# Optimization experiments

Measured on AMD Instinct MI355X. Metric: run time of the kernel, lower is better.

## Reference

```python
import jax, jax.numpy as jnp
import numpy as np


def setup_inputs() -> dict:
    key = jax.random.key(0)
    k0, k1 = jax.random.split(key)
    B, S, T = 32, 512, 128
    return {
        "crf_score_0": jax.random.normal(k0, (B, S + 1, T, T), dtype=jnp.float32),
        "crf_score_1": jax.random.normal(k1, (B, S + 1, T), dtype=jnp.float32),
        "sof": 126,
        "eof": 127,
    }


def reference(crf_score_0, crf_score_1, sof, eof):
    # crf_score_0: [B, S+1, T, T], crf_score_1: [B, S+1, T]
    # Initial scores (note: original multiplies, not adds, at step 0)
    forscores = crf_score_0[:, 0, sof, :] * crf_score_1[:, 0, :]  # [B, T]

    # Move seq axis first for scan: [S, B, T, T] and [S, B, T]
    c0 = jnp.moveaxis(crf_score_0[:, 1:], 0, 1)
    c1 = jnp.moveaxis(crf_score_1[:, 1:], 0, 1)

    def fwd_step(fs, xs):
        t0, t1 = xs  # [B, T, T], [B, T]
        # cur[b, i, j] = fs[b, i] + t1[b, j] + t0[b, i, j]
        cur = fs[:, :, None] + t1[:, None, :] + t0
        new_fs = jnp.max(cur, axis=1)            # [B, T]
        bp = jnp.argmax(cur, axis=1).astype(jnp.int32)  # [B, T]
        return new_fs, bp

    _, back_points = jax.lax.scan(fwd_step, forscores, (c0, c1))  # bps: [S, B, T]

    # Backtrack exactly as the original loop: pointer starts at bp[-1][:, eof],
    # then for idx = S-1 .. 0: pointer = bp[idx][b, pointer]; decode[:, idx] = pointer.
    ptr0 = back_points[-1][:, eof]  # [B]

    def bwd_step(ptr, bp_t):
        new = jnp.take_along_axis(bp_t, ptr[:, None], axis=1)[:, 0]
        return new, new

    _, dec = jax.lax.scan(bwd_step, ptr0, back_points, reverse=True)  # [S, B]
    return dec.T.astype(jnp.int32)  # [B, S] decoded label indices
```

## Files before the change

kernel.cpp:

```cpp
#include <hip/hip_runtime.h>


constexpr int S = 512;
constexpr int T = 128;

__global__ __launch_bounds__(1024, 1)
void viterbi_fused(const float* __restrict__ c0, const float* __restrict__ c1,
                   const int* __restrict__ sofp, const int* __restrict__ eofp,
                   int* __restrict__ out)
{
    __shared__ float fs[2][T];
    __shared__ float pmax[32][T];
    __shared__ int   parg[32][T];
    __shared__ unsigned char bp[S][T];

    const int b   = blockIdx.x;
    const int tid = (int)threadIdx.x;
    const int jq  = tid & 31;
    const int g   = tid >> 5;
    const int col = jq * 4;
    const int row = g * 4;

    const float* c0b = c0 + (size_t)b * (S + 1) * T * T;
    const float* c1b = c1 + (size_t)b * (S + 1) * T;

    if (tid < T) {
        const int sof = sofp[0];
        fs[0][tid] = c0b[(size_t)sof * T + tid] * c1b[tid];
    }
    __syncthreads();

    {
    }
    const float* t0p = c0b + (size_t)1 * T * T;
    const float* t1p = c1b + (size_t)1 * T;
    float4 a0 = *(const float4*)(t0p + (size_t)(row + 0) * T + col);
    float4 a1 = *(const float4*)(t0p + (size_t)(row + 1) * T + col);
    float4 a2 = *(const float4*)(t0p + (size_t)(row + 2) * T + col);
    float4 a3 = *(const float4*)(t0p + (size_t)(row + 3) * T + col);
    float4 tv = *(const float4*)(t1p + col);

    int p = 0;
    for (int s = 1; s <= S; ++s) {
        float4 b0 = make_float4(0.f,0.f,0.f,0.f), b1 = b0, b2 = b0, b3 = b0, bt = b0;
        if (s < S) {
            const float* n0 = c0b + (size_t)(s + 1) * T * T;
            const float* n1 = c1b + (size_t)(s + 1) * T;
            b0 = *(const float4*)(n0 + (size_t)(row + 0) * T + col);
            b1 = *(const float4*)(n0 + (size_t)(row + 1) * T + col);
            b2 = *(const float4*)(n0 + (size_t)(row + 2) * T + col);
            b3 = *(const float4*)(n0 + (size_t)(row + 3) * T + col);
            bt = *(const float4*)(n1 + col);
        }

        const float f0 = fs[p][row + 0];
        const float f1 = fs[p][row + 1];
        const float f2 = fs[p][row + 2];
        const float f3 = fs[p][row + 3];

        float bx, by, bz, bw; int ix, iy, iz, iw; float v;
        bx = (f0 + tv.x) + a0.x; ix = row;
        by = (f0 + tv.y) + a0.y; iy = row;
        bz = (f0 + tv.z) + a0.z; iz = row;
        bw = (f0 + tv.w) + a0.w; iw = row;

        v = (f1 + tv.x) + a1.x; if (v > bx) { bx = v; ix = row + 1; }
        v = (f1 + tv.y) + a1.y; if (v > by) { by = v; iy = row + 1; }
        v = (f1 + tv.z) + a1.z; if (v > bz) { bz = v; iz = row + 1; }
        v = (f1 + tv.w) + a1.w; if (v > bw) { bw = v; iw = row + 1; }

        v = (f2 + tv.x) + a2.x; if (v > bx) { bx = v; ix = row + 2; }
        v = (f2 + tv.y) + a2.y; if (v > by) { by = v; iy = row + 2; }
        v = (f2 + tv.z) + a2.z; if (v > bz) { bz = v; iz = row + 2; }
        v = (f2 + tv.w) + a2.w; if (v > bw) { bw = v; iw = row + 2; }

        v = (f3 + tv.x) + a3.x; if (v > bx) { bx = v; ix = row + 3; }
        v = (f3 + tv.y) + a3.y; if (v > by) { by = v; iy = row + 3; }
        v = (f3 + tv.z) + a3.z; if (v > bz) { bz = v; iz = row + 3; }
        v = (f3 + tv.w) + a3.w; if (v > bw) { bw = v; iw = row + 3; }

        *(float4*)&pmax[g][col] = make_float4(bx, by, bz, bw);
        *(int4*)  &parg[g][col] = make_int4(ix, iy, iz, iw);
        __syncthreads();

        if (tid < T) {
            float bb = pmax[0][tid];
            int   ii = parg[0][tid];
            #pragma unroll
            for (int gg = 1; gg < 32; ++gg) {
                float vv = pmax[gg][tid];
                if (vv > bb) { bb = vv; ii = parg[gg][tid]; }
            }
            fs[p ^ 1][tid] = bb;
            bp[s - 1][tid] = (unsigned char)ii;
        }
        __syncthreads();

        p ^= 1;
        a0 = b0; a1 = b1; a2 = b2; a3 = b3; tv = bt;
    }

    if (tid == 0) {
        const int eof = eofp[0];
        int ptr = bp[S - 1][eof];
        for (int idx = S - 1; idx >= 0; --idx) {
            ptr = bp[idx][ptr];
            out[(size_t)b * S + idx] = ptr;
        }
    }
}

extern "C" void kernel_launch(void* const* d_in, const int* in_sizes, int n_in,
                              void* d_out, int out_size, void* d_ws, size_t ws_size,
                              hipStream_t stream)
{
    const float* c0  = (const float*)d_in[0];
    const float* c1  = (const float*)d_in[1];
    const int*   sof = (const int*)d_in[2];
    const int*   eof = (const int*)d_in[3];
    int*         out = (int*)d_out;

    const int B = in_sizes[1] / ((S + 1) * T);
    viterbi_fused<<<dim3(B), dim3(1024), 0, stream>>>(c0, c1, sof, eof, out);
}
```

Before: 849.4 us.

## Prefetch two steps ahead, pre-reduce with wave shuffles, use lighter barriers

Result: faster. 821.8 us (-3.2%).

```diff
diff --git a/kernel.cpp b/kernel.cpp
--- a/kernel.cpp
+++ b/kernel.cpp
@@ -3,6 +3,11 @@
 
 constexpr int S = 512;
 constexpr int T = 128;
+
+__device__ __forceinline__ void bar_lds() {
+    asm volatile("s_waitcnt lgkmcnt(0)" ::: "memory");
+    __builtin_amdgcn_s_barrier();
+}
 
 __global__ __launch_bounds__(1024, 1)
 void viterbi_fused(const float* __restrict__ c0, const float* __restrict__ c1,
@@ -10,16 +15,18 @@
                    int* __restrict__ out)
 {
     __shared__ float fs[2][T];
-    __shared__ float pmax[32][T];
-    __shared__ int   parg[32][T];
+    __shared__ float pmax[16][T];
+    __shared__ int   parg[16][T];
     __shared__ unsigned char bp[S][T];
 
-    const int b   = blockIdx.x;
-    const int tid = (int)threadIdx.x;
-    const int jq  = tid & 31;
-    const int g   = tid >> 5;
-    const int col = jq * 4;
-    const int row = g * 4;
+    const int b    = blockIdx.x;
+    const int tid  = (int)threadIdx.x;
+    const int lane = tid & 63;
+    const int w    = tid >> 6;
+    const int jq   = lane & 31;
+    const int g    = tid >> 5;
+    const int col  = jq * 4;
+    const int row  = g * 4;
 
     const float* c0b = c0 + (size_t)b * (S + 1) * T * T;
     const float* c1b = c1 + (size_t)b * (S + 1) * T;
@@ -28,31 +35,28 @@
         const int sof = sofp[0];
         fs[0][tid] = c0b[(size_t)sof * T + tid] * c1b[tid];
     }
-    __syncthreads();
 
+    float4 A0, A1, A2, A3, At, B0, B1, B2, B3, Bt;
     {
+        const float* t0p = c0b + (size_t)1 * T * T;
+        A0 = *(const float4*)(t0p + (size_t)(row + 0) * T + col);
+        A1 = *(const float4*)(t0p + (size_t)(row + 1) * T + col);
+        A2 = *(const float4*)(t0p + (size_t)(row + 2) * T + col);
+        A3 = *(const float4*)(t0p + (size_t)(row + 3) * T + col);
+        At = *(const float4*)(c1b + (size_t)1 * T + col);
+        const float* u0p = c0b + (size_t)2 * T * T;
+        B0 = *(const float4*)(u0p + (size_t)(row + 0) * T + col);
+        B1 = *(const float4*)(u0p + (size_t)(row + 1) * T + col);
+        B2 = *(const float4*)(u0p + (size_t)(row + 2) * T + col);
+        B3 = *(const float4*)(u0p + (size_t)(row + 3) * T + col);
+        Bt = *(const float4*)(c1b + (size_t)2 * T + col);
     }
-    const float* t0p = c0b + (size_t)1 * T * T;
-    const float* t1p = c1b + (size_t)1 * T;
-    float4 a0 = *(const float4*)(t0p + (size_t)(row + 0) * T + col);
-    float4 a1 = *(const float4*)(t0p + (size_t)(row + 1) * T + col);
-    float4 a2 = *(const float4*)(t0p + (size_t)(row + 2) * T + col);
-    float4 a3 = *(const float4*)(t0p + (size_t)(row + 3) * T + col);
-    float4 tv = *(const float4*)(t1p + col);
+    bar_lds();
 
     int p = 0;
-    for (int s = 1; s <= S; ++s) {
-        float4 b0 = make_float4(0.f,0.f,0.f,0.f), b1 = b0, b2 = b0, b3 = b0, bt = b0;
-        if (s < S) {
-            const float* n0 = c0b + (size_t)(s + 1) * T * T;
-            const float* n1 = c1b + (size_t)(s + 1) * T;
-            b0 = *(const float4*)(n0 + (size_t)(row + 0) * T + col);
-            b1 = *(const float4*)(n0 + (size_t)(row + 1) * T + col);
-            b2 = *(const float4*)(n0 + (size_t)(row + 2) * T + col);
-            b3 = *(const float4*)(n0 + (size_t)(row + 3) * T + col);
-            bt = *(const float4*)(n1 + col);
-        }
 
+    auto STEP = [&](int s, float4& a0, float4& a1, float4& a2, float4& a3,
+                    float4& tv) {
         const float f0 = fs[p][row + 0];
         const float f1 = fs[p][row + 1];
         const float f2 = fs[p][row + 2];
@@ -79,25 +83,51 @@
         v = (f3 + tv.z) + a3.z; if (v > bz) { bz = v; iz = row + 3; }
         v = (f3 + tv.w) + a3.w; if (v > bw) { bw = v; iw = row + 3; }
 
-        *(float4*)&pmax[g][col] = make_float4(bx, by, bz, bw);
-        *(int4*)  &parg[g][col] = make_int4(ix, iy, iz, iw);
-        __syncthreads();
+        if (s + 2 <= S) {
+            const float* n0 = c0b + (size_t)(s + 2) * T * T;
+            a0 = *(const float4*)(n0 + (size_t)(row + 0) * T + col);
+            a1 = *(const float4*)(n0 + (size_t)(row + 1) * T + col);
+            a2 = *(const float4*)(n0 + (size_t)(row + 2) * T + col);
+            a3 = *(const float4*)(n0 + (size_t)(row + 3) * T + col);
+            tv = *(const float4*)(c1b + (size_t)(s + 2) * T + col);
+        }
+
+        float cx = __shfl_xor(bx, 32, 64);
+        float cy = __shfl_xor(by, 32, 64);
+        float cz = __shfl_xor(bz, 32, 64);
+        float cw = __shfl_xor(bw, 32, 64);
+        int   dx = __shfl_xor(ix, 32, 64);
+        int   dy = __shfl_xor(iy, 32, 64);
+        int   dz = __shfl_xor(iz, 32, 64);
+        int   dw = __shfl_xor(iw, 32, 64);
+        if (lane < 32) {
+            if (cx > bx) { bx = cx; ix = dx; }
+            if (cy > by) { by = cy; iy = dy; }
+            if (cz > bz) { bz = cz; iz = dz; }
+            if (cw > bw) { bw = cw; iw = dw; }
+            *(float4*)&pmax[w][col] = make_float4(bx, by, bz, bw);
+            *(int4*)  &parg[w][col] = make_int4(ix, iy, iz, iw);
+        }
+        bar_lds();
 
         if (tid < T) {
             float bb = pmax[0][tid];
             int   ii = parg[0][tid];
             #pragma unroll
-            for (int gg = 1; gg < 32; ++gg) {
+            for (int gg = 1; gg < 16; ++gg) {
                 float vv = pmax[gg][tid];
                 if (vv > bb) { bb = vv; ii = parg[gg][tid]; }
             }
             fs[p ^ 1][tid] = bb;
             bp[s - 1][tid] = (unsigned char)ii;
         }
-        __syncthreads();
+        bar_lds();
+        p ^= 1;
+    };
 
-        p ^= 1;
-        a0 = b0; a1 = b1; a2 = b2; a3 = b3; tv = bt;
+    for (int s = 1; s <= S; s += 2) {
+        STEP(s,     A0, A1, A2, A3, At);
+        STEP(s + 1, B0, B1, B2, B3, Bt);
     }
 
     if (tid == 0) {
```

## Double-buffer global prefetch two steps ahead, pack value/index, split reduction chains

Applied to the files above, without the earlier changes.

Result: slower. 968.6 us (+14.0%).

```diff
diff --git a/kernel.cpp b/kernel.cpp
--- a/kernel.cpp
+++ b/kernel.cpp
@@ -3,6 +3,15 @@
 
 constexpr int S = 512;
 constexpr int T = 128;
+
+__device__ __forceinline__ void bar_lds() {
+    asm volatile("s_waitcnt lgkmcnt(0)" ::: "memory");
+    __builtin_amdgcn_s_barrier();
+}
+
+__device__ __forceinline__ unsigned long long pack_vi(float v, int i) {
+    return ((unsigned long long)__float_as_uint(v) << 32) | (unsigned int)i;
+}
 
 __global__ __launch_bounds__(1024, 1)
 void viterbi_fused(const float* __restrict__ c0, const float* __restrict__ c1,
@@ -10,8 +19,7 @@
                    int* __restrict__ out)
 {
     __shared__ float fs[2][T];
-    __shared__ float pmax[32][T];
-    __shared__ int   parg[32][T];
+    __shared__ unsigned long long part[32][T];
     __shared__ unsigned char bp[S][T];
 
     const int b   = blockIdx.x;
@@ -28,31 +36,29 @@
         const int sof = sofp[0];
         fs[0][tid] = c0b[(size_t)sof * T + tid] * c1b[tid];
     }
-    __syncthreads();
 
-    {
-    }
-    const float* t0p = c0b + (size_t)1 * T * T;
-    const float* t1p = c1b + (size_t)1 * T;
-    float4 a0 = *(const float4*)(t0p + (size_t)(row + 0) * T + col);
-    float4 a1 = *(const float4*)(t0p + (size_t)(row + 1) * T + col);
-    float4 a2 = *(const float4*)(t0p + (size_t)(row + 2) * T + col);
-    float4 a3 = *(const float4*)(t0p + (size_t)(row + 3) * T + col);
-    float4 tv = *(const float4*)(t1p + col);
+    const float* pA = c0b + (size_t)T * T + (size_t)row * T + col;
+    const float* qA = c1b + T + col;
+    const float* pB = pA + T * T;
+    const float* qB = qA + T;
+
+    float4 A0 = *(const float4*)(pA);
+    float4 A1 = *(const float4*)(pA + T);
+    float4 A2 = *(const float4*)(pA + 2 * T);
+    float4 A3 = *(const float4*)(pA + 3 * T);
+    float4 At = *(const float4*)(qA);
+    float4 B0 = *(const float4*)(pB);
+    float4 B1 = *(const float4*)(pB + T);
+    float4 B2 = *(const float4*)(pB + 2 * T);
+    float4 B3 = *(const float4*)(pB + 3 * T);
+    float4 Bt = *(const float4*)(qB);
+
+    bar_lds();
 
     int p = 0;
-    for (int s = 1; s <= S; ++s) {
-        float4 b0 = make_float4(0.f,0.f,0.f,0.f), b1 = b0, b2 = b0, b3 = b0, bt = b0;
-        if (s < S) {
-            const float* n0 = c0b + (size_t)(s + 1) * T * T;
-            const float* n1 = c1b + (size_t)(s + 1) * T;
-            b0 = *(const float4*)(n0 + (size_t)(row + 0) * T + col);
-            b1 = *(const float4*)(n0 + (size_t)(row + 1) * T + col);
-            b2 = *(const float4*)(n0 + (size_t)(row + 2) * T + col);
-            b3 = *(const float4*)(n0 + (size_t)(row + 3) * T + col);
-            bt = *(const float4*)(n1 + col);
-        }
 
+    auto STEP = [&](int s, float4& a0, float4& a1, float4& a2, float4& a3,
+                    float4& tv, const float*& pp, const float*& qq) {
         const float f0 = fs[p][row + 0];
         const float f1 = fs[p][row + 1];
         const float f2 = fs[p][row + 2];
@@ -79,25 +85,81 @@
         v = (f3 + tv.z) + a3.z; if (v > bz) { bz = v; iz = row + 3; }
         v = (f3 + tv.w) + a3.w; if (v > bw) { bw = v; iw = row + 3; }
 
-        *(float4*)&pmax[g][col] = make_float4(bx, by, bz, bw);
-        *(int4*)  &parg[g][col] = make_int4(ix, iy, iz, iw);
-        __syncthreads();
+        if (s + 2 <= S) {
+            pp += 2 * T * T;
+            qq += 2 * T;
+            a0 = *(const float4*)(pp);
+            a1 = *(const float4*)(pp + T);
+            a2 = *(const float4*)(pp + 2 * T);
+            a3 = *(const float4*)(pp + 3 * T);
+            tv = *(const float4*)(qq);
+        }
+
+        ulonglong2 w0, w1;
+        w0.x = pack_vi(bx, ix);
+        w0.y = pack_vi(by, iy);
+        w1.x = pack_vi(bz, iz);
+        w1.y = pack_vi(bw, iw);
+        *(ulonglong2*)&part[g][col]     = w0;
+        *(ulonglong2*)&part[g][col + 2] = w1;
+        bar_lds();
 
         if (tid < T) {
-            float bb = pmax[0][tid];
-            int   ii = parg[0][tid];
-            #pragma unroll
-            for (int gg = 1; gg < 32; ++gg) {
-                float vv = pmax[gg][tid];
-                if (vv > bb) { bb = vv; ii = parg[gg][tid]; }
+            float v0, v1c, v2c, v3c; int i0, i1c, i2c, i3c;
+            {
+                unsigned long long k = part[0][tid];
+                v0 = __uint_as_float((unsigned)(k >> 32)); i0 = (int)(unsigned)k;
+                #pragma unroll
+                for (int gg = 1; gg < 8; ++gg) {
+                    unsigned long long c = part[gg][tid];
+                    float vv = __uint_as_float((unsigned)(c >> 32));
+                    if (vv > v0) { v0 = vv; i0 = (int)(unsigned)c; }
+                }
             }
-            fs[p ^ 1][tid] = bb;
-            bp[s - 1][tid] = (unsigned char)ii;
+            {
+                unsigned long long k = part[8][tid];
+                v1c = __uint_as_float((unsigned)(k >> 32)); i1c = (int)(unsigned)k;
+                #pragma unroll
+                for (int gg = 9; gg < 16; ++gg) {
+                    unsigned long long c = part[gg][tid];
+                    float vv = __uint_as_float((unsigned)(c >> 32));
+                    if (vv > v1c) { v1c = vv; i1c = (int)(unsigned)c; }
+                }
+            }
+            {
+                unsigned long long k = part[16][tid];
+                v2c = __uint_as_float((unsigned)(k >> 32)); i2c = (int)(unsigned)k;
+                #pragma unroll
+                for (int gg = 17; gg < 24; ++gg) {
+                    unsigned long long c = part[gg][tid];
+                    float vv = __uint_as_float((unsigned)(c >> 32));
+                    if (vv > v2c) { v2c = vv; i2c = (int)(unsigned)c; }
+                }
+            }
+            {
+                unsigned long long k = part[24][tid];
+                v3c = __uint_as_float((unsigned)(k >> 32)); i3c = (int)(unsigned)k;
+                #pragma unroll
+                for (int gg = 25; gg < 32; ++gg) {
+                    unsigned long long c = part[gg][tid];
+                    float vv = __uint_as_float((unsigned)(c >> 32));
+                    if (vv > v3c) { v3c = vv; i3c = (int)(unsigned)c; }
+                }
+            }
+            if (v1c > v0) { v0 = v1c; i0 = i1c; }
+            if (v2c > v0) { v0 = v2c; i0 = i2c; }
+            if (v3c > v0) { v0 = v3c; i0 = i3c; }
+
+            fs[p ^ 1][tid] = v0;
+            bp[s - 1][tid] = (unsigned char)i0;
         }
-        __syncthreads();
+        bar_lds();
+        p ^= 1;
+    };
 
-        p ^= 1;
-        a0 = b0; a1 = b1; a2 = b2; a3 = b3; tv = bt;
+    for (int s = 1; s <= S; s += 2) {
+        STEP(s,     A0, A1, A2, A3, At, pA, qA);
+        STEP(s + 1, B0, B1, B2, B3, Bt, pB, qB);
     }
 
     if (tid == 0) {
```

## Split each batch's Viterbi forward across eight workgroups with global-memory step handoff

Applied to the files above, without the earlier changes.

Result: faster. 697.8 us (-17.8%).

```diff
diff --git a/kernel.cpp b/kernel.cpp
--- a/kernel.cpp
+++ b/kernel.cpp
@@ -1,18 +1,180 @@
 #include <hip/hip_runtime.h>
 
 
-constexpr int S = 512;
-constexpr int T = 128;
+constexpr int S    = 512;
+constexpr int T    = 128;
+constexpr int NSL  = 8;
+constexpr int ROWS = T / NSL;
+
+__device__ __forceinline__ void bar_lds() {
+    asm volatile("s_waitcnt lgkmcnt(0)" ::: "memory");
+    __builtin_amdgcn_s_barrier();
+}
+
+__device__ __forceinline__ unsigned long long pack_vi(float v, int i) {
+    return ((unsigned long long)__float_as_uint(v) << 32) | (unsigned int)i;
+}
+__device__ __forceinline__ float hi_f(unsigned long long m) {
+    return __uint_as_float((unsigned)(m >> 32));
+}
+
+__global__ __launch_bounds__(256, 1)
+void viterbi_fwd(const float* __restrict__ c0, const float* __restrict__ c1,
+                 const int* __restrict__ sofp,
+                 unsigned long long* __restrict__ pub,
+                 unsigned char* __restrict__ bp)
+{
+    __shared__ float fsl[ROWS];
+    __shared__ unsigned long long part[8][T];
+
+    const int g    = blockIdx.x;
+    const int b    = g & 31;
+    const int k    = g >> 5;
+    const int tid  = (int)threadIdx.x;
+    const int r    = tid >> 5;
+    const int c    = tid & 31;
+    const int j0   = c * 4;
+    const int row0 = k * ROWS;
+    const int iA   = row0 + 2 * r;
+    const int iB   = iA + 1;
+
+    const float* c0b = c0 + (size_t)b * (S + 1) * T * T;
+    const float* c1b = c1 + (size_t)b * (S + 1) * T;
+    unsigned long long* pubB = pub + (size_t)b * 2 * NSL * T;
+
+    if (tid < ROWS) {
+        const int sof = sofp[0];
+        fsl[tid] = c0b[(size_t)sof * T + row0 + tid] * c1b[row0 + tid];
+    }
+
+    const float* pA = c0b + (size_t)T * T + (size_t)iA * T + j0;
+    const float* qA = c1b + T + j0;
+    const float* pB = pA + T * T;
+    const float* qB = qA + T;
+
+    float4 A0 = *(const float4*)(pA);
+    float4 A1 = *(const float4*)(pA + T);
+    float4 At = *(const float4*)(qA);
+    float4 B0 = *(const float4*)(pB);
+    float4 B1 = *(const float4*)(pB + T);
+    float4 Bt = *(const float4*)(qB);
+
+    bar_lds();
+
+    auto STEP = [&](int s, float4& a0, float4& a1, float4& tv,
+                    const float*& pp, const float*& qq) {
+        const float f0 = fsl[2 * r];
+        const float f1 = fsl[2 * r + 1];
+
+        float bx, by, bz, bw; int ix, iy, iz, iw; float v;
+        bx = (f0 + tv.x) + a0.x; ix = iA;
+        by = (f0 + tv.y) + a0.y; iy = iA;
+        bz = (f0 + tv.z) + a0.z; iz = iA;
+        bw = (f0 + tv.w) + a0.w; iw = iA;
+        v = (f1 + tv.x) + a1.x; if (v > bx) { bx = v; ix = iB; }
+        v = (f1 + tv.y) + a1.y; if (v > by) { by = v; iy = iB; }
+        v = (f1 + tv.z) + a1.z; if (v > bz) { bz = v; iz = iB; }
+        v = (f1 + tv.w) + a1.w; if (v > bw) { bw = v; iw = iB; }
+
+        if (s + 2 <= S) {
+            pp += 2 * T * T;
+            qq += 2 * T;
+            a0 = *(const float4*)(pp);
+            a1 = *(const float4*)(pp + T);
+            tv = *(const float4*)(qq);
+        }
+
+        ulonglong2 w0, w1;
+        w0.x = pack_vi(bx, ix); w0.y = pack_vi(by, iy);
+        w1.x = pack_vi(bz, iz); w1.y = pack_vi(bw, iw);
+        *(ulonglong2*)&part[r][j0]     = w0;
+        *(ulonglong2*)&part[r][j0 + 2] = w1;
+        bar_lds();
+
+        if (tid < T) {
+            unsigned long long m = part[0][tid];
+            float mv = hi_f(m);
+            #pragma unroll
+            for (int rr = 1; rr < 8; ++rr) {
+                unsigned long long cnd = part[rr][tid];
+                float cv = hi_f(cnd);
+                if (cv > mv) { mv = cv; m = cnd; }
+            }
+            unsigned long long payload =
+                (m & 0xffffffff00000000ull) |
+                (unsigned)(((unsigned)s << 8) | (unsigned)(m & 0xffu));
+            __hip_atomic_store(&pubB[(size_t)((s & 1) * NSL + k) * T + tid],
+                               payload, __ATOMIC_RELAXED,
+                               __HIP_MEMORY_SCOPE_AGENT);
+        }
+
+        if (tid < ROWS) {
+            const unsigned long long* ps =
+                pubB + (size_t)(s & 1) * NSL * T + (row0 + tid);
+            unsigned long long cand[8];
+            for (;;) {
+                bool ok = true;
+                #pragma unroll
+                for (int sl = 0; sl < 8; ++sl)
+                    cand[sl] = __hip_atomic_load(ps + sl * T, __ATOMIC_RELAXED,
+                                                 __HIP_MEMORY_SCOPE_AGENT);
+                #pragma unroll
+                for (int sl = 0; sl < 8; ++sl)
+                    ok &= (((unsigned)cand[sl] >> 8) == (unsigned)s);
+                if (ok) break;
+            }
+            unsigned long long m = cand[0];
+            float mv = hi_f(m);
+            #pragma unroll
+            for (int sl = 1; sl < 8; ++sl) {
+                float cv = hi_f(cand[sl]);
+                if (cv > mv) { mv = cv; m = cand[sl]; }
+            }
+            fsl[tid] = mv;
+            bp[((size_t)b * S + (s - 1)) * T + row0 + tid] =
+                (unsigned char)(m & 0xffu);
+        }
+        bar_lds();
+    };
+
+    for (int s = 1; s <= S; s += 2) {
+        STEP(s,     A0, A1, At, pA, qA);
+        STEP(s + 1, B0, B1, Bt, pB, qB);
+    }
+}
 
 __global__ __launch_bounds__(1024, 1)
-void viterbi_fused(const float* __restrict__ c0, const float* __restrict__ c1,
-                   const int* __restrict__ sofp, const int* __restrict__ eofp,
-                   int* __restrict__ out)
+void viterbi_bwd(const unsigned char* __restrict__ bp,
+                 const int* __restrict__ eofp, int* __restrict__ out)
+{
+    __shared__ unsigned char lbp[S][T];
+    const int b   = blockIdx.x;
+    const int tid = (int)threadIdx.x;
+
+    const uint4* s4 = (const uint4*)(bp + (size_t)b * S * T);
+    uint4* d4 = (uint4*)&lbp[0][0];
+    #pragma unroll
+    for (int it = 0; it < 4; ++it) d4[tid + it * 1024] = s4[tid + it * 1024];
+    __syncthreads();
+
+    if (tid == 0) {
+        int ptr = lbp[S - 1][eofp[0]];
+        for (int idx = S - 1; idx >= 0; --idx) {
+            ptr = lbp[idx][ptr];
+            out[(size_t)b * S + idx] = ptr;
+        }
+    }
+}
+
+__global__ __launch_bounds__(1024, 1)
+void viterbi_fused_fb(const float* __restrict__ c0, const float* __restrict__ c1,
+                      const int* __restrict__ sofp, const int* __restrict__ eofp,
+                      int* __restrict__ out)
 {
     __shared__ float fs[2][T];
     __shared__ float pmax[32][T];
     __shared__ int   parg[32][T];
-    __shared__ unsigned char bp[S][T];
+    __shared__ unsigned char bpl[S][T];
 
     const int b   = blockIdx.x;
     const int tid = (int)threadIdx.x;
@@ -30,29 +192,24 @@
     }
     __syncthreads();
 
-    {
-    }
-    const float* t0p = c0b + (size_t)1 * T * T;
-    const float* t1p = c1b + (size_t)1 * T;
+    const float* t0p = c0b + (size_t)T * T;
     float4 a0 = *(const float4*)(t0p + (size_t)(row + 0) * T + col);
     float4 a1 = *(const float4*)(t0p + (size_t)(row + 1) * T + col);
     float4 a2 = *(const float4*)(t0p + (size_t)(row + 2) * T + col);
     float4 a3 = *(const float4*)(t0p + (size_t)(row + 3) * T + col);
-    float4 tv = *(const float4*)(t1p + col);
+    float4 tv = *(const float4*)(c1b + T + col);
 
     int p = 0;
     for (int s = 1; s <= S; ++s) {
         float4 b0 = make_float4(0.f,0.f,0.f,0.f), b1 = b0, b2 = b0, b3 = b0, bt = b0;
         if (s < S) {
             const float* n0 = c0b + (size_t)(s + 1) * T * T;
-            const float* n1 = c1b + (size_t)(s + 1) * T;
             b0 = *(const float4*)(n0 + (size_t)(row + 0) * T + col);
             b1 = *(const float4*)(n0 + (size_t)(row + 1) * T + col);
             b2 = *(const float4*)(n0 + (size_t)(row + 2) * T + col);
             b3 = *(const float4*)(n0 + (size_t)(row + 3) * T + col);
-            bt = *(const float4*)(n1 + col);
-        }
-
+            bt = *(const float4*)(c1b + (size_t)(s + 1) * T + col);
+        }
         const float f0 = fs[p][row + 0];
         const float f1 = fs[p][row + 1];
         const float f2 = fs[p][row + 2];
@@ -63,17 +220,14 @@
         by = (f0 + tv.y) + a0.y; iy = row;
         bz = (f0 + tv.z) + a0.z; iz = row;
         bw = (f0 + tv.w) + a0.w; iw = row;
-
         v = (f1 + tv.x) + a1.x; if (v > bx) { bx = v; ix = row + 1; }
         v = (f1 + tv.y) + a1.y; if (v > by) { by = v; iy = row + 1; }
         v = (f1 + tv.z) + a1.z; if (v > bz) { bz = v; iz = row + 1; }
         v = (f1 + tv.w) + a1.w; if (v > bw) { bw = v; iw = row + 1; }
-
         v = (f2 + tv.x) + a2.x; if (v > bx) { bx = v; ix = row + 2; }
         v = (f2 + tv.y) + a2.y; if (v > by) { by = v; iy = row + 2; }
         v = (f2 + tv.z) + a2.z; if (v > bz) { bz = v; iz = row + 2; }
         v = (f2 + tv.w) + a2.w; if (v > bw) { bw = v; iw = row + 2; }
-
         v = (f3 + tv.x) + a3.x; if (v > bx) { bx = v; ix = row + 3; }
         v = (f3 + tv.y) + a3.y; if (v > by) { by = v; iy = row + 3; }
         v = (f3 + tv.z) + a3.z; if (v > bz) { bz = v; iz = row + 3; }
@@ -92,19 +246,18 @@
                 if (vv > bb) { bb = vv; ii = parg[gg][tid]; }
             }
             fs[p ^ 1][tid] = bb;
-            bp[s - 1][tid] = (unsigned char)ii;
+            bpl[s - 1][tid] = (unsigned char)ii;
         }
         __syncthreads();
-
         p ^= 1;
         a0 = b0; a1 = b1; a2 = b2; a3 = b3; tv = bt;
     }
 
     if (tid == 0) {
         const int eof = eofp[0];
-        int ptr = bp[S - 1][eof];
+        int ptr = bpl[S - 1][eof];
         for (int idx = S - 1; idx >= 0; --idx) {
-            ptr = bp[idx][ptr];
+            ptr = bpl[idx][ptr];
             out[(size_t)b * S + idx] = ptr;
         }
     }
@@ -121,5 +274,15 @@
     int*         out = (int*)d_out;
 
     const int B = in_sizes[1] / ((S + 1) * T);
-    viterbi_fused<<<dim3(B), dim3(1024), 0, stream>>>(c0, c1, sof, eof, out);
-}
+
+    const size_t pub_bytes = (size_t)B * 2 * NSL * T * 8;
+    const size_t bp_bytes  = (size_t)B * S * T;
+    if (ws_size >= pub_bytes + bp_bytes) {
+        unsigned long long* pub = (unsigned long long*)d_ws;
+        unsigned char* bp = (unsigned char*)d_ws + pub_bytes;
+        viterbi_fwd<<<dim3(B * NSL), dim3(256), 0, stream>>>(c0, c1, sof, pub, bp);
+        viterbi_bwd<<<dim3(B), dim3(1024), 0, stream>>>(bp, eof, out);
+    } else {
+        viterbi_fused_fb<<<dim3(B), dim3(1024), 0, stream>>>(c0, c1, sof, eof, out);
+    }
+}
```
